# Performance work log

Hardware: AMD Instinct MI355X
Metric: run time of the kernel (lower is better)

Reference implementation:

```python
import jax, jax.numpy as jnp
from jax import lax
import numpy as np

ANCHOR_MASK = [[6, 7, 8], [3, 4, 5], [0, 1, 2]]
MODEL_INPUT = (416.0, 416.0)  # (H, W)
IGNORE_THRESH = 0.5
MAX_BOXES = 32


def setup_inputs() -> dict:
    rng = np.random.default_rng(0)
    B, NC, A = 16, 80, 3
    C = 5 + NC
    out = {}
    for l, g in enumerate([13, 26, 52]):
        p = rng.uniform(0.02, 0.98, size=(B, g, g, A, C)).astype(np.float32)
        p[..., 2:4] = rng.normal(0.0, 0.5, size=(B, g, g, A, 2)).astype(np.float32)
        t = np.zeros((B, g, g, A, C), np.float32)
        for b in range(B):
            n = 20
            gy = rng.integers(0, g, n)
            gx = rng.integers(0, g, n)
            a = rng.integers(0, A, n)
            xy = (np.stack([gx, gy], -1) + rng.uniform(0.0, 1.0, (n, 2))) / g
            wh = rng.uniform(0.05, 0.5, (n, 2))
            cls = rng.integers(0, NC, n)
            t[b, gy, gx, a, 0:2] = xy
            t[b, gy, gx, a, 2:4] = wh
            t[b, gy, gx, a, 4] = 1.0
            t[b, gy, gx, a, 5 + cls] = 1.0
        out[f"pred{l}"] = jnp.asarray(p)
        out[f"tgt{l}"] = jnp.asarray(t)
    out["anchors"] = jnp.asarray(
        [[10, 13], [16, 30], [33, 23], [30, 61], [62, 45], [59, 119],
         [116, 90], [156, 198], [373, 326]], dtype=jnp.float32)
    return out


def _bce(p, t):
    # elementwise binary cross-entropy, matches nn.BCELoss(reduction='none')
    return -(t * jnp.log(p) + (1.0 - t) * jnp.log1p(-p))


def _layer_loss(pred, tgt, anc):
    # pred, tgt: [B,H,W,A,5+NC]; anc: [A,2] (w,h)
    B, H, W, A, C = pred.shape
    dt = pred.dtype
    gs_flip = jnp.array([W, H], dtype=dt)            # flipped grid shape (w,h)
    mis_flip = jnp.array([MODEL_INPUT[1], MODEL_INPUT[0]], dtype=dt)
    gy, gx = jnp.meshgrid(jnp.arange(H, dtype=dt), jnp.arange(W, dtype=dt), indexing='ij')
    grid = jnp.stack([gx, gy], axis=-1)[:, :, None, :]   # [H,W,1,2]

    obj = tgt[..., 4:5]                                   # [B,H,W,A,1]
    scale = 2.0 - tgt[..., 2:3] * tgt[..., 3:4]

    raw_t_xy = tgt[..., 0:2] * gs_flip - grid[None]
    twh = tgt[..., 2:4] * mis_flip / anc                  # [B,H,W,A,2]
    nz = twh != 0
    raw_t_wh = jnp.where(nz, jnp.log(jnp.where(nz, twh, 1.0)), 0.0)

    pred_xy = (pred[..., 0:2] + grid[None]) / gs_flip
    pred_wh = jnp.exp(pred[..., 2:4]) * anc / mis_flip

    # --- ignore mask: IoU of each prediction vs (padded) valid target boxes ---
    obj_flat = obj[..., 0].reshape(B, -1)                 # [B, H*W*A]
    vals, idx = lax.top_k(obj_flat, MAX_BOXES)            # [B,K]
    boxes = tgt[..., 0:4].reshape(B, -1, 4)
    sel = jnp.take_along_axis(boxes, idx[..., None], axis=1)  # [B,K,4]
    t_xy = sel[..., 0:2][:, None, None, None]             # [B,1,1,1,K,2]
    t_wh = sel[..., 2:4][:, None, None, None]
    p_xy = pred_xy[..., None, :]                          # [B,H,W,A,1,2]
    p_wh = pred_wh[..., None, :]
    mins = jnp.maximum(p_xy - p_wh / 2, t_xy - t_wh / 2)
    maxs = jnp.minimum(p_xy + p_wh / 2, t_xy + t_wh / 2)
    iwh = jnp.clip(maxs - mins, 0.0)
    inter = iwh[..., 0] * iwh[..., 1]                     # [B,H,W,A,K]
    p_area = p_wh[..., 0] * p_wh[..., 1]
    t_area = t_wh[..., 0] * t_wh[..., 1]
    iou = inter / (p_area + t_area - inter)
    iou = iou * (vals[:, None, None, None, :] > 0).astype(dt)  # zero padded slots
    max_iou = jnp.max(iou, axis=-1, keepdims=True)        # [B,H,W,A,1]
    ignore = (max_iou < IGNORE_THRESH).astype(dt)

    xy_loss = _bce(pred[..., 0:2], raw_t_xy) * scale * obj
    wh_loss = 0.5 * jnp.square(pred[..., 2:4] - raw_t_wh) * scale * obj
    conf_loss = _bce(pred[..., 4:5], obj) * (obj + (1.0 - obj) * ignore)
    cls_loss = _bce(pred[..., 5:], tgt[..., 5:]) * obj

    per_img = (xy_loss.sum(axis=(1, 2, 3, 4)) + wh_loss.sum(axis=(1, 2, 3, 4))
               + conf_loss.sum(axis=(1, 2, 3, 4)) + cls_loss.sum(axis=(1, 2, 3, 4)))
    return jnp.mean(per_img)


def reference(pred0, pred1, pred2, tgt0, tgt1, tgt2, anchors):
    total = jnp.zeros((), dtype=pred0.dtype)
    for l, (p, t) in enumerate([(pred0, tgt0), (pred1, tgt1), (pred2, tgt2)]):
        anc = anchors[jnp.array(ANCHOR_MASK[l])]
        total = total + _layer_loss(p, t, anc)
    return total
```

## Files before the change

kernel.cpp:

```cpp
#include <hip/hip_runtime.h>

#define CCH  85
#define N0   (16*13*13*3)
#define N1   (16*26*26*3)
#define N2   (16*52*52*3)
#define NTOT (N0+N1+N2)
#define NBLK ((NTOT + 255) / 256)
#define BPB  40
#define MAXB 32

#define FLAGS_OFF 0
#define CNT_OFF   170368
#define TAGS_OFF  173056
#define BOX_OFF   280064

typedef float v4f __attribute__((ext_vector_type(4), aligned(4)));

__device__ __forceinline__ void decode(int i, int& l, int& li, int& g) {
    if (i < N0)           { l = 0; li = i;           g = 13; }
    else if (i < N0 + N1) { l = 1; li = i - N0;      g = 26; }
    else                  { l = 2; li = i - N0 - N1; g = 52; }
}

__device__ __forceinline__ float anc_x(int l, int a) {
    if (l == 0) return (a == 0) ? 116.f : (a == 1) ? 156.f : 373.f;
    if (l == 1) return (a == 0) ?  30.f : (a == 1) ?  62.f :  59.f;
    return          (a == 0) ?  10.f : (a == 1) ?  16.f :  33.f;
}
__device__ __forceinline__ float anc_y(int l, int a) {
    if (l == 0) return (a == 0) ?  90.f : (a == 1) ? 198.f : 326.f;
    if (l == 1) return (a == 0) ?  61.f : (a == 1) ?  45.f : 119.f;
    return          (a == 0) ?  13.f : (a == 1) ?  30.f :  23.f;
}

__device__ __forceinline__ int lb_of(int gi) {
    int ll, lli, gg;
    decode(gi, ll, lli, gg);
    return ll * 16 + lli / (gg * gg * 3);
}

__global__ void __launch_bounds__(256) k1_scan(
        const float* __restrict__ t0, const float* __restrict__ t1,
        const float* __restrict__ t2,
        unsigned char* __restrict__ flags,
        int* __restrict__ counts_priv, int* __restrict__ tags_priv,
        float4* __restrict__ boxes_priv, float* __restrict__ out) {
    int bid = blockIdx.x;
    int tid = threadIdx.x;
    int i = bid * 256 + tid;
    bool valid = i < NTOT;

    int l = 0, li = 0, g = 13;
    if (valid) decode(i, l, li, g);
    const float* T = (l == 0) ? t0 : (l == 1) ? t1 : t2;
    size_t base = (size_t)li * CCH;

    float obj = 0.0f;
    if (valid) obj = T[base + 4];
    if (valid) flags[i] = (obj > 0.0f) ? 1 : 0;

    __shared__ int cnt;
    __shared__ float4 lbox[BPB];
    __shared__ int llb[BPB];
    if (tid == 0) cnt = 0;
    __syncthreads();

    if (valid && obj > 0.0f) {
        int cpi = g * g * 3;
        int b = li / cpi;
        int pos = atomicAdd(&cnt, 1);
        if (pos < BPB) {
            v4f tb4 = *(const v4f*)(T + base);
            lbox[pos] = make_float4(tb4.x, tb4.y, tb4.z, tb4.w);
            llb[pos]  = l * 16 + b;
        }
    }
    __syncthreads();

    int n = cnt < BPB ? cnt : BPB;
    if (tid == 0) counts_priv[bid] = n;
    if (tid < n) {
        boxes_priv[bid * BPB + tid] = lbox[tid];
        tags_priv[bid * BPB + tid]  = llb[tid];
    }
    if (bid == 0 && tid == 0) out[0] = 0.0f;
}

__global__ void __launch_bounds__(256) k2_loss(
        const float* __restrict__ p0, const float* __restrict__ t0,
        const float* __restrict__ p1, const float* __restrict__ t1,
        const float* __restrict__ p2, const float* __restrict__ t2,
        const unsigned char* __restrict__ flags,
        const int* __restrict__ counts_priv, const int* __restrict__ tags_priv,
        const float4* __restrict__ boxes_priv, float* __restrict__ out) {
    int bid = blockIdx.x;
    int tid = threadIdx.x;
    int i = bid * 256 + tid;
    bool valid = i < NTOT;

    int l = 0, li = 0, g = 13;
    if (valid) decode(i, l, li, g);
    const float* P = (l == 0) ? p0 : (l == 1) ? p1 : p2;
    const float* T = (l == 0) ? t0 : (l == 1) ? t1 : t2;
    size_t base = (size_t)li * CCH;

    v4f pv4 = {0.5f, 0.5f, 0.0f, 0.0f};
    float pc = 0.5f;
    int flag = 0;
    if (valid) {
        pv4 = *(const v4f*)(P + base);
        pc  = P[base + 4];
        flag = flags[i];
    }

    int cpi = g * g * 3;
    int b = li / cpi;
    int c = li % cpi;
    int a = c % 3;
    int w = (c / 3) % g;
    int h = c / (3 * g);
    int lb = l * 16 + b;

    int iLast = (bid * 256 + 255 < NTOT) ? bid * 256 + 255 : NTOT - 1;
    int lbA = lb_of(bid * 256);
    int lbB = lb_of(iLast);

    __shared__ float4 sbox[2][MAXB];
    __shared__ int scnt[2];
    if (tid < 2) scnt[tid] = 0;
    __syncthreads();

    auto gather = [&](int lbT, int listIdx, int tbase) {
        int lT = lbT >> 4, bT = lbT & 15;
        int Ls, cpiT;
        if (lT == 0)      { Ls = 0;       cpiT = 13 * 13 * 3; }
        else if (lT == 1) { Ls = N0;      cpiT = 26 * 26 * 3; }
        else              { Ls = N0 + N1; cpiT = 52 * 52 * 3; }
        int jstart = (Ls + bT * cpiT) >> 8;
        int jend   = (Ls + (bT + 1) * cpiT - 1) >> 8;
        int t = tid - tbase;
        if (t >= 0 && t <= jend - jstart) {
            int j = jstart + t;
            int cj = counts_priv[j];
            if (cj > BPB) cj = BPB;
            for (int k = 0; k < cj; ++k) {
                if (tags_priv[j * BPB + k] == lbT) {
                    int p = atomicAdd(&scnt[listIdx], 1);
                    if (p < MAXB) sbox[listIdx][p] = boxes_priv[j * BPB + k];
                }
            }
        }
    };
    gather(lbA, 0, 0);
    if (lbB != lbA) gather(lbB, 1, 128);
    __syncthreads();

    float acc = 0.0f;
    int lane = tid & 63, wid = tid >> 6;

    if (valid) {
        if (flag) {
            acc = -__logf(pc);
        } else {
            float ax = anc_x(l, a), ay = anc_y(l, a);
            float gf = (float)g;
            float pxn = (pv4.x + (float)w) / gf;
            float pyn = (pv4.y + (float)h) / gf;
            float pwn = __expf(pv4.z) * ax * (1.0f / 416.0f);
            float phn = __expf(pv4.w) * ay * (1.0f / 416.0f);
            float pl = pxn - pwn * 0.5f, pr = pxn + pwn * 0.5f;
            float pt = pyn - phn * 0.5f, pb = pyn + phn * 0.5f;
            float p_area = pwn * phn;
            int listIdx = (lb == lbA) ? 0 : 1;
            int cntL = scnt[listIdx];
            if (cntL > MAXB) cntL = MAXB;
            const float4* bx = sbox[listIdx];
            float maxiou = 0.0f;
            #pragma unroll 4
            for (int k = 0; k < cntL; ++k) {
                float4 tb = bx[k];
                float il = fmaxf(pl, tb.x - tb.z * 0.5f);
                float ir = fminf(pr, tb.x + tb.z * 0.5f);
                float it = fmaxf(pt, tb.y - tb.w * 0.5f);
                float ib = fminf(pb, tb.y + tb.w * 0.5f);
                float iw = fmaxf(ir - il, 0.0f);
                float ih = fmaxf(ib - it, 0.0f);
                float inter = iw * ih;
                float iou = __fdividef(inter, p_area + tb.z * tb.w - inter);
                maxiou = fmaxf(maxiou, iou);
            }
            if (maxiou < 0.5f) acc = -__logf(1.0f - pc);
        }
    }

    unsigned long long mask = __ballot(valid && flag);
    while (mask) {
        int src = __ffsll(mask) - 1;
        mask &= mask - 1;
        int l2  = __shfl(l,  src, 64);
        int li2 = __shfl(li, src, 64);
        const float *P2 = (l2 == 0) ? p0 : (l2 == 1) ? p1 : p2;
        const float *T2 = (l2 == 0) ? t0 : (l2 == 1) ? t1 : t2;
        int g2 = (l2 == 0) ? 13 : (l2 == 1) ? 26 : 52;
        int cpi2 = g2 * g2 * 3;
        int c2 = li2 % cpi2;
        int a2 = c2 % 3;
        int w2 = (c2 / 3) % g2;
        int h2 = c2 / (3 * g2);
        size_t base2 = (size_t)li2 * CCH;

        float pv = P2[base2 + lane];
        float tv = T2[base2 + lane];
        bool has2 = lane < (CCH - 64);
        float pvB = 1.0f, tvB = 1.0f;
        if (has2) { pvB = P2[base2 + 64 + lane]; tvB = T2[base2 + 64 + lane]; }

        float tx = __shfl(tv, 0, 64), ty = __shfl(tv, 1, 64);
        float tw = __shfl(tv, 2, 64), th = __shfl(tv, 3, 64);
        float qx = __shfl(pv, 0, 64), qy = __shfl(pv, 1, 64);
        float qw = __shfl(pv, 2, 64), qh = __shfl(pv, 3, 64);

        if (lane >= 5)
            acc += -(tv * __logf(pv) + (1.0f - tv) * __logf(1.0f - pv));
        if (has2)
            acc += -(tvB * __logf(pvB) + (1.0f - tvB) * __logf(1.0f - pvB));

        if (lane == 0) {
            float scale = 2.0f - tw * th;
            float gf = (float)g2;
            float rtx = tx * gf - (float)w2;
            float rty = ty * gf - (float)h2;
            float ax = anc_x(l2, a2), ay = anc_y(l2, a2);
            float rtw = __logf(tw * 416.0f / ax);
            float rth = __logf(th * 416.0f / ay);
            acc += (-(rtx * __logf(qx) + (1.0f - rtx) * __logf(1.0f - qx))) * scale;
            acc += (-(rty * __logf(qy) + (1.0f - rty) * __logf(1.0f - qy))) * scale;
            acc += 0.5f * (qw - rtw) * (qw - rtw) * scale;
            acc += 0.5f * (qh - rth) * (qh - rth) * scale;
        }
    }

    acc *= (1.0f / 16.0f);

    for (int off = 32; off > 0; off >>= 1)
        acc += __shfl_down(acc, off, 64);
    __shared__ float s[4];
    if (lane == 0) s[wid] = acc;
    __syncthreads();
    if (tid == 0)
        atomicAdd(out, s[0] + s[1] + s[2] + s[3]);
}

extern "C" void kernel_launch(void* const* d_in, const int* in_sizes, int n_in,
                              void* d_out, int out_size, void* d_ws, size_t ws_size,
                              hipStream_t stream) {
    const float* p0 = (const float*)d_in[0];
    const float* t0 = (const float*)d_in[1];
    const float* p1 = (const float*)d_in[2];
    const float* t1 = (const float*)d_in[3];
    const float* p2 = (const float*)d_in[4];
    const float* t2 = (const float*)d_in[5];

    unsigned char* flags = (unsigned char*)d_ws;
    int*    counts_priv  = (int*)((char*)d_ws + CNT_OFF);
    int*    tags_priv    = (int*)((char*)d_ws + TAGS_OFF);
    float4* boxes_priv   = (float4*)((char*)d_ws + BOX_OFF);
    float*  outp         = (float*)d_out;

    k1_scan<<<NBLK, 256, 0, stream>>>(t0, t1, t2, flags,
                                      counts_priv, tags_priv, boxes_priv, outp);
    k2_loss<<<NBLK, 256, 0, stream>>>(p0, t0, p1, t1, p2, t2, flags,
                                      counts_priv, tags_priv, boxes_priv, outp);
}
```

Measured before the change: 30.43 us.

## Move prediction decode and object losses into first kernel, leave IoU ignore pass

The first kernel now reads predictions as well as targets. It computes the positive-cell losses and decodes predicted boxes, area and negative confidence loss into a compact workspace record per cell. The second kernel only gathers target boxes and runs the IoU max test over those records. This rebalances work so the strided prediction reads happen while the scan runs, at the cost of extra workspace writes and reads (24 bytes per cell) and a memset launch to zero the output.

```diff
diff --git a/kernel.cpp b/kernel.cpp
--- a/kernel.cpp
+++ b/kernel.cpp
@@ -9,10 +9,11 @@
 #define BPB  40
 #define MAXB 32
 
-#define FLAGS_OFF 0
-#define CNT_OFF   170368
-#define TAGS_OFF  173056
-#define BOX_OFF   280064
+#define RECBOX_OFF  0
+#define RECMETA_OFF 2725632
+#define CNT_OFF     4088448
+#define TAGS_OFF    4091136
+#define BOX_OFF     4197696
 
 typedef float v4f __attribute__((ext_vector_type(4), aligned(4)));
 
@@ -39,10 +40,11 @@
     return ll * 16 + lli / (gg * gg * 3);
 }
 
-__global__ void __launch_bounds__(256) k1_scan(
-        const float* __restrict__ t0, const float* __restrict__ t1,
-        const float* __restrict__ t2,
-        unsigned char* __restrict__ flags,
+__global__ void __launch_bounds__(256) k1_gather(
+        const float* __restrict__ p0, const float* __restrict__ t0,
+        const float* __restrict__ p1, const float* __restrict__ t1,
+        const float* __restrict__ p2, const float* __restrict__ t2,
+        float4* __restrict__ recbox, float2* __restrict__ recmeta,
         int* __restrict__ counts_priv, int* __restrict__ tags_priv,
         float4* __restrict__ boxes_priv, float* __restrict__ out) {
     int bid = blockIdx.x;
@@ -52,65 +54,16 @@
 
     int l = 0, li = 0, g = 13;
     if (valid) decode(i, l, li, g);
-    const float* T = (l == 0) ? t0 : (l == 1) ? t1 : t2;
-    size_t base = (size_t)li * CCH;
-
-    float obj = 0.0f;
-    if (valid) obj = T[base + 4];
-    if (valid) flags[i] = (obj > 0.0f) ? 1 : 0;
-
-    __shared__ int cnt;
-    __shared__ float4 lbox[BPB];
-    __shared__ int llb[BPB];
-    if (tid == 0) cnt = 0;
-    __syncthreads();
-
-    if (valid && obj > 0.0f) {
-        int cpi = g * g * 3;
-        int b = li / cpi;
-        int pos = atomicAdd(&cnt, 1);
-        if (pos < BPB) {
-            v4f tb4 = *(const v4f*)(T + base);
-            lbox[pos] = make_float4(tb4.x, tb4.y, tb4.z, tb4.w);
-            llb[pos]  = l * 16 + b;
-        }
-    }
-    __syncthreads();
-
-    int n = cnt < BPB ? cnt : BPB;
-    if (tid == 0) counts_priv[bid] = n;
-    if (tid < n) {
-        boxes_priv[bid * BPB + tid] = lbox[tid];
-        tags_priv[bid * BPB + tid]  = llb[tid];
-    }
-    if (bid == 0 && tid == 0) out[0] = 0.0f;
-}
-
-__global__ void __launch_bounds__(256) k2_loss(
-        const float* __restrict__ p0, const float* __restrict__ t0,
-        const float* __restrict__ p1, const float* __restrict__ t1,
-        const float* __restrict__ p2, const float* __restrict__ t2,
-        const unsigned char* __restrict__ flags,
-        const int* __restrict__ counts_priv, const int* __restrict__ tags_priv,
-        const float4* __restrict__ boxes_priv, float* __restrict__ out) {
-    int bid = blockIdx.x;
-    int tid = threadIdx.x;
-    int i = bid * 256 + tid;
-    bool valid = i < NTOT;
-
-    int l = 0, li = 0, g = 13;
-    if (valid) decode(i, l, li, g);
     const float* P = (l == 0) ? p0 : (l == 1) ? p1 : p2;
     const float* T = (l == 0) ? t0 : (l == 1) ? t1 : t2;
     size_t base = (size_t)li * CCH;
 
     v4f pv4 = {0.5f, 0.5f, 0.0f, 0.0f};
-    float pc = 0.5f;
-    int flag = 0;
+    float pc = 0.5f, obj = 0.0f;
     if (valid) {
         pv4 = *(const v4f*)(P + base);
         pc  = P[base + 4];
-        flag = flags[i];
+        obj = T[base + 4];
     }
 
     int cpi = g * g * 3;
@@ -121,6 +74,122 @@
     int h = c / (3 * g);
     int lb = l * 16 + b;
 
+    bool isobj = valid && obj > 0.0f;
+
+    __shared__ int cnt;
+    __shared__ float4 lbox[BPB];
+    __shared__ int llb[BPB];
+    if (tid == 0) cnt = 0;
+    __syncthreads();
+    if (isobj) {
+        int pos = atomicAdd(&cnt, 1);
+        if (pos < BPB) {
+            v4f tb4 = *(const v4f*)(T + base);
+            lbox[pos] = make_float4(tb4.x, tb4.y, tb4.z, tb4.w);
+            llb[pos]  = lb;
+        }
+    }
+    __syncthreads();
+    int n = cnt < BPB ? cnt : BPB;
+    if (tid == 0) counts_priv[bid] = n;
+    if (tid < n) {
+        boxes_priv[bid * BPB + tid] = lbox[tid];
+        tags_priv[bid * BPB + tid]  = llb[tid];
+    }
+
+    float4 rbox = make_float4(0.f, 0.f, 0.f, 0.f);
+    float2 rmeta = make_float2(0.f, 0.f);
+    if (valid && !isobj) {
+        float ax = anc_x(l, a), ay = anc_y(l, a);
+        float gf = (float)g;
+        float pxn = (pv4.x + (float)w) / gf;
+        float pyn = (pv4.y + (float)h) / gf;
+        float pwn = __expf(pv4.z) * ax * (1.0f / 416.0f);
+        float phn = __expf(pv4.w) * ay * (1.0f / 416.0f);
+        rbox = make_float4(pxn - pwn * 0.5f, pxn + pwn * 0.5f,
+                           pyn - phn * 0.5f, pyn + phn * 0.5f);
+        rmeta = make_float2(pwn * phn, -__logf(1.0f - pc));
+    }
+    if (valid) {
+        recbox[i]  = rbox;
+        recmeta[i] = rmeta;
+    }
+
+    float acc = 0.0f;
+    int lane = tid & 63, wid = tid >> 6;
+    if (isobj) acc = -__logf(pc);
+
+    unsigned long long mask = __ballot(isobj);
+    while (mask) {
+        int src = __ffsll(mask) - 1;
+        mask &= mask - 1;
+        int l2  = __shfl(l,  src, 64);
+        int li2 = __shfl(li, src, 64);
+        const float *P2 = (l2 == 0) ? p0 : (l2 == 1) ? p1 : p2;
+        const float *T2 = (l2 == 0) ? t0 : (l2 == 1) ? t1 : t2;
+        int g2 = (l2 == 0) ? 13 : (l2 == 1) ? 26 : 52;
+        int cpi2 = g2 * g2 * 3;
+        int c2 = li2 % cpi2;
+        int a2 = c2 % 3;
+        int w2 = (c2 / 3) % g2;
+        int h2 = c2 / (3 * g2);
+        size_t base2 = (size_t)li2 * CCH;
+
+        float pv = P2[base2 + lane];
+        float tv = T2[base2 + lane];
+        bool has2 = lane < (CCH - 64);
+        float pvB = 1.0f, tvB = 1.0f;
+        if (has2) { pvB = P2[base2 + 64 + lane]; tvB = T2[base2 + 64 + lane]; }
+
+        float tx = __shfl(tv, 0, 64), ty = __shfl(tv, 1, 64);
+        float tw = __shfl(tv, 2, 64), th = __shfl(tv, 3, 64);
+        float qx = __shfl(pv, 0, 64), qy = __shfl(pv, 1, 64);
+        float qw = __shfl(pv, 2, 64), qh = __shfl(pv, 3, 64);
+
+        if (lane >= 5)
+            acc += -(tv * __logf(pv) + (1.0f - tv) * __logf(1.0f - pv));
+        if (has2)
+            acc += -(tvB * __logf(pvB) + (1.0f - tvB) * __logf(1.0f - pvB));
+
+        if (lane == 0) {
+            float scale = 2.0f - tw * th;
+            float gf = (float)g2;
+            float rtx = tx * gf - (float)w2;
+            float rty = ty * gf - (float)h2;
+            float ax = anc_x(l2, a2), ay = anc_y(l2, a2);
+            float rtw = __logf(tw * 416.0f / ax);
+            float rth = __logf(th * 416.0f / ay);
+            acc += (-(rtx * __logf(qx) + (1.0f - rtx) * __logf(1.0f - qx))) * scale;
+            acc += (-(rty * __logf(qy) + (1.0f - rty) * __logf(1.0f - qy))) * scale;
+            acc += 0.5f * (qw - rtw) * (qw - rtw) * scale;
+            acc += 0.5f * (qh - rth) * (qh - rth) * scale;
+        }
+    }
+
+    acc *= (1.0f / 16.0f);
+    for (int off = 32; off > 0; off >>= 1)
+        acc += __shfl_down(acc, off, 64);
+    __shared__ float s[4];
+    if (lane == 0) s[wid] = acc;
+    __syncthreads();
+    if (tid == 0)
+        atomicAdd(out, s[0] + s[1] + s[2] + s[3]);
+}
+
+__global__ void __launch_bounds__(256) k2_ignore(
+        const float4* __restrict__ recbox, const float2* __restrict__ recmeta,
+        const int* __restrict__ counts_priv, const int* __restrict__ tags_priv,
+        const float4* __restrict__ boxes_priv, float* __restrict__ out) {
+    int bid = blockIdx.x;
+    int tid = threadIdx.x;
+    int i = bid * 256 + tid;
+    bool valid = i < NTOT;
+
+    float4 rbox = make_float4(0.f, 0.f, 0.f, 0.f);
+    float2 rmeta = make_float2(0.f, 0.f);
+    if (valid) { rbox = recbox[i]; rmeta = recmeta[i]; }
+
+    int lb = valid ? lb_of(i) : 0;
     int iLast = (bid * 256 + 255 < NTOT) ? bid * 256 + 255 : NTOT - 1;
     int lbA = lb_of(bid * 256);
     int lbB = lb_of(iLast);
@@ -156,95 +225,35 @@
     __syncthreads();
 
     float acc = 0.0f;
-    int lane = tid & 63, wid = tid >> 6;
-
     if (valid) {
-        if (flag) {
-            acc = -__logf(pc);
-        } else {
-            float ax = anc_x(l, a), ay = anc_y(l, a);
-            float gf = (float)g;
-            float pxn = (pv4.x + (float)w) / gf;
-            float pyn = (pv4.y + (float)h) / gf;
-            float pwn = __expf(pv4.z) * ax * (1.0f / 416.0f);
-            float phn = __expf(pv4.w) * ay * (1.0f / 416.0f);
-            float pl = pxn - pwn * 0.5f, pr = pxn + pwn * 0.5f;
-            float pt = pyn - phn * 0.5f, pb = pyn + phn * 0.5f;
-            float p_area = pwn * phn;
-            int listIdx = (lb == lbA) ? 0 : 1;
-            int cntL = scnt[listIdx];
-            if (cntL > MAXB) cntL = MAXB;
-            const float4* bx = sbox[listIdx];
-            float maxiou = 0.0f;
-            #pragma unroll 4
-            for (int k = 0; k < cntL; ++k) {
-                float4 tb = bx[k];
-                float il = fmaxf(pl, tb.x - tb.z * 0.5f);
-                float ir = fminf(pr, tb.x + tb.z * 0.5f);
-                float it = fmaxf(pt, tb.y - tb.w * 0.5f);
-                float ib = fminf(pb, tb.y + tb.w * 0.5f);
-                float iw = fmaxf(ir - il, 0.0f);
-                float ih = fmaxf(ib - it, 0.0f);
-                float inter = iw * ih;
-                float iou = __fdividef(inter, p_area + tb.z * tb.w - inter);
-                maxiou = fmaxf(maxiou, iou);
-            }
-            if (maxiou < 0.5f) acc = -__logf(1.0f - pc);
-        }
-    }
-
-    unsigned long long mask = __ballot(valid && flag);
-    while (mask) {
-        int src = __ffsll(mask) - 1;
-        mask &= mask - 1;
-        int l2  = __shfl(l,  src, 64);
-        int li2 = __shfl(li, src, 64);
-        const float *P2 = (l2 == 0) ? p0 : (l2 == 1) ? p1 : p2;
-        const float *T2 = (l2 == 0) ? t0 : (l2 == 1) ? t1 : t2;
-        int g2 = (l2 == 0) ? 13 : (l2 == 1) ? 26 : 52;
-        int cpi2 = g2 * g2 * 3;
-        int c2 = li2 % cpi2;
-        int a2 = c2 % 3;
-        int w2 = (c2 / 3) % g2;
-        int h2 = c2 / (3 * g2);
-        size_t base2 = (size_t)li2 * CCH;
-
-        float pv = P2[base2 + lane];
-        float tv = T2[base2 + lane];
-        bool has2 = lane < (CCH - 64);
-        float pvB = 1.0f, tvB = 1.0f;
-        if (has2) { pvB = P2[base2 + 64 + lane]; tvB = T2[base2 + 64 + lane]; }
-
-        float tx = __shfl(tv, 0, 64), ty = __shfl(tv, 1, 64);
-        float tw = __shfl(tv, 2, 64), th = __shfl(tv, 3, 64);
-        float qx = __shfl(pv, 0, 64), qy = __shfl(pv, 1, 64);
-        float qw = __shfl(pv, 2, 64), qh = __shfl(pv, 3, 64);
-
-        if (lane >= 5)
-            acc += -(tv * __logf(pv) + (1.0f - tv) * __logf(1.0f - pv));
-        if (has2)
-            acc += -(tvB * __logf(pvB) + (1.0f - tvB) * __logf(1.0f - pvB));
-
-        if (lane == 0) {
-            float scale = 2.0f - tw * th;
-            float gf = (float)g2;
-            float rtx = tx * gf - (float)w2;
-            float rty = ty * gf - (float)h2;
-            float ax = anc_x(l2, a2), ay = anc_y(l2, a2);
-            float rtw = __logf(tw * 416.0f / ax);
-            float rth = __logf(th * 416.0f / ay);
-            acc += (-(rtx * __logf(qx) + (1.0f - rtx) * __logf(1.0f - qx))) * scale;
-            acc += (-(rty * __logf(qy) + (1.0f - rty) * __logf(1.0f - qy))) * scale;
-            acc += 0.5f * (qw - rtw) * (qw - rtw) * scale;
-            acc += 0.5f * (qh - rth) * (qh - rth) * scale;
-        }
+        int listIdx = (lb == lbA) ? 0 : 1;
+        int cntL = scnt[listIdx];
+        if (cntL > MAXB) cntL = MAXB;
+        const float4* bx = sbox[listIdx];
+        float pl = rbox.x, pr = rbox.y, pt = rbox.z, pb = rbox.w;
+        float p_area = rmeta.x;
+        float maxiou = 0.0f;
+        #pragma unroll 4
+        for (int k = 0; k < cntL; ++k) {
+            float4 tb = bx[k];
+            float il = fmaxf(pl, tb.x - tb.z * 0.5f);
+            float ir = fminf(pr, tb.x + tb.z * 0.5f);
+            float it = fmaxf(pt, tb.y - tb.w * 0.5f);
+            float ib = fminf(pb, tb.y + tb.w * 0.5f);
+            float iw = fmaxf(ir - il, 0.0f);
+            float ih = fmaxf(ib - it, 0.0f);
+            float inter = iw * ih;
+            float iou = __fdividef(inter, p_area + tb.z * tb.w - inter);
+            maxiou = fmaxf(maxiou, iou);
+        }
+        if (maxiou < 0.5f) acc = rmeta.y;
     }
 
     acc *= (1.0f / 16.0f);
-
     for (int off = 32; off > 0; off >>= 1)
         acc += __shfl_down(acc, off, 64);
     __shared__ float s[4];
+    int lane = tid & 63, wid = tid >> 6;
     if (lane == 0) s[wid] = acc;
     __syncthreads();
     if (tid == 0)
@@ -261,14 +270,18 @@
     const float* p2 = (const float*)d_in[4];
     const float* t2 = (const float*)d_in[5];
 
-    unsigned char* flags = (unsigned char*)d_ws;
-    int*    counts_priv  = (int*)((char*)d_ws + CNT_OFF);
-    int*    tags_priv    = (int*)((char*)d_ws + TAGS_OFF);
-    float4* boxes_priv   = (float4*)((char*)d_ws + BOX_OFF);
-    float*  outp         = (float*)d_out;
-
-    k1_scan<<<NBLK, 256, 0, stream>>>(t0, t1, t2, flags,
-                                      counts_priv, tags_priv, boxes_priv, outp);
-    k2_loss<<<NBLK, 256, 0, stream>>>(p0, t0, p1, t1, p2, t2, flags,
-                                      counts_priv, tags_priv, boxes_priv, outp);
-}
+    float4* recbox      = (float4*)((char*)d_ws + RECBOX_OFF);
+    float2* recmeta     = (float2*)((char*)d_ws + RECMETA_OFF);
+    int*    counts_priv = (int*)((char*)d_ws + CNT_OFF);
+    int*    tags_priv   = (int*)((char*)d_ws + TAGS_OFF);
+    float4* boxes_priv  = (float4*)((char*)d_ws + BOX_OFF);
+    float*  outp        = (float*)d_out;
+
+    (void)hipMemsetAsync(d_out, 0, sizeof(float), stream);
+
+    k1_gather<<<NBLK, 256, 0, stream>>>(p0, t0, p1, t1, p2, t2,
+                                        recbox, recmeta,
+                                        counts_priv, tags_priv, boxes_priv, outp);
+    k2_ignore<<<NBLK, 256, 0, stream>>>(recbox, recmeta,
+                                        counts_priv, tags_priv, boxes_priv, outp);
+}
```

Result: slower. 42.98 us (+41.3%).

## Stream pred blocks coalesced into LDS and extract first five channels

Applied to the files above, without the earlier changes.

The loss kernel now has each block cooperatively read its whole contiguous slice of the prediction tensor with aligned 16-byte vector loads. Only channels 0-4 (box and confidence) are scattered into a channel-major LDS buffer, and each thread then reads its values from LDS. This replaces per-thread strided loads at 340-byte spacing with fully coalesced loads, but it reads all 85 channels per cell instead of just 5. It also adds per-element divide-by-85 index math and an extra LDS buffer. The vector type alignment is raised to 16, and the scan kernel's box load becomes scalar to stay legal for unaligned addresses.

```diff
diff --git a/kernel.cpp b/kernel.cpp
--- a/kernel.cpp
+++ b/kernel.cpp
@@ -14,7 +14,7 @@
 #define TAGS_OFF  173056
 #define BOX_OFF   280064
 
-typedef float v4f __attribute__((ext_vector_type(4), aligned(4)));
+typedef float v4f __attribute__((ext_vector_type(4), aligned(16)));
 
 __device__ __forceinline__ void decode(int i, int& l, int& li, int& g) {
     if (i < N0)           { l = 0; li = i;           g = 13; }
@@ -70,8 +70,8 @@
         int b = li / cpi;
         int pos = atomicAdd(&cnt, 1);
         if (pos < BPB) {
-            v4f tb4 = *(const v4f*)(T + base);
-            lbox[pos] = make_float4(tb4.x, tb4.y, tb4.z, tb4.w);
+            lbox[pos] = make_float4(T[base + 0], T[base + 1],
+                                    T[base + 2], T[base + 3]);
             llb[pos]  = l * 16 + b;
         }
     }
@@ -86,7 +86,7 @@
     if (bid == 0 && tid == 0) out[0] = 0.0f;
 }
 
-__global__ void __launch_bounds__(256) k2_loss(
+__global__ void __launch_bounds__(256) k2_stream(
         const float* __restrict__ p0, const float* __restrict__ t0,
         const float* __restrict__ p1, const float* __restrict__ t1,
         const float* __restrict__ p2, const float* __restrict__ t2,
@@ -98,21 +98,47 @@
     int i = bid * 256 + tid;
     bool valid = i < NTOT;
 
+    __shared__ float lds_pred[5 * 256];
+    __shared__ float4 sbox[2][MAXB];
+    __shared__ int scnt[2];
+    if (tid < 2) scnt[tid] = 0;
+    __syncthreads();
+
+    {
+        const int layerStart[4] = {0, N0, N0 + N1, NTOT};
+        const float* PL[3] = {p0, p1, p2};
+        int i0 = bid * 256;
+        int i1 = i0 + 256 < NTOT ? i0 + 256 : NTOT;
+        #pragma unroll
+        for (int lsg = 0; lsg < 3; ++lsg) {
+            int s = i0 > layerStart[lsg] ? i0 : layerStart[lsg];
+            int e = i1 < layerStart[lsg + 1] ? i1 : layerStart[lsg + 1];
+            if (s >= e) continue;
+            const float* P = PL[lsg];
+            int li0 = s - layerStart[lsg];
+            int lofs = s - i0;
+            unsigned f0 = (unsigned)li0 * 85u;
+            unsigned f1 = (unsigned)(li0 + (e - s)) * 85u;
+            int w0 = (int)(f0 >> 2);
+            int w1 = (int)((f1 + 3u) >> 2);
+            for (int w = w0 + tid; w < w1; w += 256) {
+                v4f q = *(const v4f*)(P + ((size_t)w << 2));
+                #pragma unroll
+                for (int el = 0; el < 4; ++el) {
+                    unsigned f = ((unsigned)w << 2) + el;
+                    if (f >= f0 && f < f1) {
+                        unsigned c  = __umulhi(f, 3233857729u) >> 6;
+                        unsigned ch = f - c * 85u;
+                        if (ch < 5u)
+                            lds_pred[ch * 256 + (c - (unsigned)li0) + lofs] = q[el];
+                    }
+                }
+            }
+        }
+    }
+
     int l = 0, li = 0, g = 13;
     if (valid) decode(i, l, li, g);
-    const float* P = (l == 0) ? p0 : (l == 1) ? p1 : p2;
-    const float* T = (l == 0) ? t0 : (l == 1) ? t1 : t2;
-    size_t base = (size_t)li * CCH;
-
-    v4f pv4 = {0.5f, 0.5f, 0.0f, 0.0f};
-    float pc = 0.5f;
-    int flag = 0;
-    if (valid) {
-        pv4 = *(const v4f*)(P + base);
-        pc  = P[base + 4];
-        flag = flags[i];
-    }
-
     int cpi = g * g * 3;
     int b = li / cpi;
     int c = li % cpi;
@@ -121,14 +147,12 @@
     int h = c / (3 * g);
     int lb = l * 16 + b;
 
+    int flag = 0;
+    if (valid) flag = flags[i];
+
     int iLast = (bid * 256 + 255 < NTOT) ? bid * 256 + 255 : NTOT - 1;
     int lbA = lb_of(bid * 256);
     int lbB = lb_of(iLast);
-
-    __shared__ float4 sbox[2][MAXB];
-    __shared__ int scnt[2];
-    if (tid < 2) scnt[tid] = 0;
-    __syncthreads();
 
     auto gather = [&](int lbT, int listIdx, int tbase) {
         int lT = lbT >> 4, bT = lbT & 15;
@@ -155,19 +179,22 @@
     if (lbB != lbA) gather(lbB, 1, 128);
     __syncthreads();
 
+    float px = lds_pred[tid],        py = lds_pred[256 + tid];
+    float pw = lds_pred[512 + tid],  ph = lds_pred[768 + tid];
+    float pc = lds_pred[1024 + tid];
+
     float acc = 0.0f;
     int lane = tid & 63, wid = tid >> 6;
-
     if (valid) {
         if (flag) {
             acc = -__logf(pc);
         } else {
             float ax = anc_x(l, a), ay = anc_y(l, a);
             float gf = (float)g;
-            float pxn = (pv4.x + (float)w) / gf;
-            float pyn = (pv4.y + (float)h) / gf;
-            float pwn = __expf(pv4.z) * ax * (1.0f / 416.0f);
-            float phn = __expf(pv4.w) * ay * (1.0f / 416.0f);
+            float pxn = (px + (float)w) / gf;
+            float pyn = (py + (float)h) / gf;
+            float pwn = __expf(pw) * ax * (1.0f / 416.0f);
+            float phn = __expf(ph) * ay * (1.0f / 416.0f);
             float pl = pxn - pwn * 0.5f, pr = pxn + pwn * 0.5f;
             float pt = pyn - phn * 0.5f, pb = pyn + phn * 0.5f;
             float p_area = pwn * phn;
@@ -269,6 +296,6 @@
 
     k1_scan<<<NBLK, 256, 0, stream>>>(t0, t1, t2, flags,
                                       counts_priv, tags_priv, boxes_priv, outp);
-    k2_loss<<<NBLK, 256, 0, stream>>>(p0, t0, p1, t1, p2, t2, flags,
-                                      counts_priv, tags_priv, boxes_priv, outp);
-}
+    k2_stream<<<NBLK, 256, 0, stream>>>(p0, t0, p1, t1, p2, t2, flags,
+                                        counts_priv, tags_priv, boxes_priv, outp);
+}
```

Result: slower. 37.48 us (+23.2%).
